# Kernel optimization log

Hardware: AMD Instinct MI355X
Metric: run time of the kernel (lower is better)

Reference implementation:

```python
import jax, jax.numpy as jnp
import numpy as np

IMG_DIM = 28 * 28


def _distmat(X):
    # D[i,j] = ||x_i||^2 - 2 x_i.x_j + ||x_j||^2
    r = jnp.sum(X * X, axis=1)
    a = X @ X.T
    return r[:, None] - 2.0 * a + r[None, :]


def _sigma_from_self(D, m):
    """Replicates sigma_estimation(X, X): median of the strict lower triangle of
    distmat(cat([X, X])), which is the 2x2 block-tiled matrix [[D,D],[D,D]].
    Its strict lower triangle multiset = full D (block 2,1) + 2x strict tril(D).
    Clamps: if med<=0 use mean; floor at 0.01. Detached (stop_gradient), matching
    the torch .detach().cpu().numpy() path."""
    mask = jnp.tril(jnp.ones((m, m), dtype=bool), -1)
    tril_inf = jnp.where(mask, D, jnp.inf)
    vals = jnp.concatenate([D.ravel(), tril_inf.ravel(), tril_inf.ravel()])
    s = jnp.sort(vals)  # inf padding sorts to the end
    k = 2 * m * m - m  # number of strict-lower-triangle entries of a 2m x 2m matrix
    if k % 2 == 0:
        med = 0.5 * (s[k // 2 - 1] + s[k // 2])  # np.median averages middles
    else:
        med = s[(k - 1) // 2]
    tri_sum = jnp.sum(jnp.where(mask, D, 0.0))
    mean_tri = (jnp.sum(D) + 2.0 * tri_sum) / k
    med = jnp.where(med <= 0.0, mean_tri, med)
    med = jnp.maximum(med, 0.01)
    return jax.lax.stop_gradient(med)


def _centered_kernel(D, sigma):
    # Kxc = Kx @ (I - ones/m)  ==  Kx - rowmean(Kx)
    K = jnp.exp(-D / (2.0 * sigma * sigma))
    return K - jnp.mean(K, axis=1, keepdims=True)


def _hsic_norm_from_kernels(Kxc, Kyc):
    Pxy = jnp.mean(Kxc * Kyc.T)
    Px = jnp.sqrt(jnp.mean(Kxc * Kxc.T))
    Py = jnp.sqrt(jnp.mean(Kyc * Kyc.T))
    return Pxy / (Px * Py)


def reference(x, y):
    x2 = x.reshape((-1, IMG_DIM))  # [m, 784]
    m = x2.shape[0]
    d = y.shape[-1]

    # hsic_normalized(x, y) with per-variable median sigma
    Dx = _distmat(x2)
    Dy = _distmat(y)
    Kx = _centered_kernel(Dx, _sigma_from_self(Dx, m))
    Ky = _centered_kernel(Dy, _sigma_from_self(Dy, m))
    mi_io = _hsic_norm_from_kernels(Kx, Ky)

    # Batched version of the nested loop over latent component pairs (i<j).
    # Per-column 1-D distance matrices: [d, m, m]
    yt = y.T  # [d, m]
    Dc = (yt[:, :, None] - yt[:, None, :]) ** 2
    sig = jax.vmap(lambda D: _sigma_from_self(D, m))(Dc)  # [d]
    Kc = jnp.exp(-Dc / (2.0 * sig * sig)[:, None, None])
    Kc = Kc - jnp.mean(Kc, axis=2, keepdims=True)  # centered, [d, m, m]

    # P[a,b] = mean(K_a * K_b^T)
    P = jnp.einsum('aij,bji->ab', Kc, Kc) / (m * m)
    diag = jnp.diagonal(P)
    norm = P / jnp.sqrt(diag[:, None] * diag[None, :])
    pair_mask = jnp.triu(jnp.ones((d, d), dtype=bool), 1)  # i < j
    mi_component_sum = jnp.sum(jnp.where(pair_mask, norm, 0.0))

    return -mi_io + mi_component_sum


def setup_inputs() -> dict:
    key = jax.random.key(0)
    kx, ky = jax.random.split(key)
    x = jax.random.normal(kx, (2048, 784), dtype=jnp.float32)
    y = jax.random.normal(ky, (2048, 10), dtype=jnp.float32)
    return {"x": x, "y": y}
```

## Files before the change

### kernel.cpp

```cpp
#include <hip/hip_runtime.h>
#include <math.h>

constexpr int Md   = 2048;
constexpr int NDIM = 784;
constexpr int DYC  = 10;
constexpr int MM   = Md * Md;
constexpr unsigned RANK_LO = 4193279u;
constexpr unsigned RANK_HI = 4193280u;
constexpr int NPROB = 12;
constexpr int NB    = 128;
constexpr int NBINS = 8192;

constexpr size_t OFF_DX     = 0;
constexpr size_t OFF_DY     = OFF_DX + (size_t)MM * 4;
constexpr size_t OFF_RX     = OFF_DY + (size_t)MM * 4;
constexpr size_t OFF_RY     = OFF_RX + Md * 8;
constexpr size_t OFF_RC     = OFF_RY + Md * 8;
constexpr size_t OFF_GACC   = OFF_RC + (size_t)DYC * Md * 8;
constexpr size_t OFF_HISTA  = OFF_GACC + 64 * 8;
constexpr size_t OFF_HISTB  = OFF_HISTA + (size_t)NPROB * NBINS * 4;
constexpr size_t OFF_JOBS   = OFF_HISTB + (size_t)NPROB * NBINS * 4;
constexpr size_t OFF_SELKEY = OFF_JOBS + NPROB * 5 * 4;
constexpr size_t OFF_Q      = OFF_SELKEY + NPROB * 2 * 4;
constexpr size_t OFF_RXN    = OFF_Q + NPROB * 4;
constexpr size_t OFF_YT     = OFF_RXN + Md * 4;
constexpr size_t OFF_RES    = OFF_YT + (size_t)DYC * Md * 4;
constexpr size_t WS_NEED    = OFF_RES + 70 * 8;
constexpr size_t ZERO_BASE  = OFF_GACC;
constexpr size_t ZERO_LEN   = OFF_JOBS - OFF_GACC;

typedef _Float16 f16x8 __attribute__((ext_vector_type(8)));
typedef _Float16 f16x4 __attribute__((ext_vector_type(4)));
typedef float    f32x16 __attribute__((ext_vector_type(16)));

__device__ __forceinline__ unsigned fkey(float v) {
  unsigned u = __float_as_uint(v);
  return (u & 0x80000000u) ? ~u : (u | 0x80000000u);
}
__device__ __forceinline__ float keyinv(unsigned k) {
  unsigned u = (k & 0x80000000u) ? (k ^ 0x80000000u) : ~k;
  return __uint_as_float(u);
}
__device__ __forceinline__ f16x8 ld8(const _Float16* p) {
  f16x4 lo = *(const f16x4*)p;
  f16x4 hi = *(const f16x4*)(p + 4);
  f16x8 r;
  r[0]=lo[0]; r[1]=lo[1]; r[2]=lo[2]; r[3]=lo[3];
  r[4]=hi[0]; r[5]=hi[1]; r[6]=hi[2]; r[7]=hi[3];
  return r;
}
__device__ __forceinline__ double waveReduceD(double v) {
  #pragma unroll
  for (int o = 32; o > 0; o >>= 1) v += __shfl_down(v, o, 64);
  return v;
}

__device__ __forceinline__ double blockReduceD(double v) {
  __shared__ double sred[4];
  v = waveReduceD(v);
  int lane = threadIdx.x & 63;
  int w    = threadIdx.x >> 6;
  __syncthreads();
  if (lane == 0) sred[w] = v;
  __syncthreads();
  double r = 0.0;
  if (threadIdx.x == 0) { r = sred[0] + sred[1] + sred[2] + sred[3]; }
  return r;
}

__global__ void fail_kernel(float* out) { if (threadIdx.x == 0) out[0] = 0.0f; }

__global__ void init_jobs_kernel(unsigned* __restrict__ jobs) {
  int p = threadIdx.x;
  if (p < NPROB) {
    jobs[p * 5 + 0] = 0u;
    jobs[p * 5 + 1] = RANK_LO;
    jobs[p * 5 + 2] = 0u;
    jobs[p * 5 + 3] = RANK_HI;
    jobs[p * 5 + 4] = 0u;
  }
}

__global__ __launch_bounds__(256) void transpose_y_kernel(const float* __restrict__ Y,
                                                          float* __restrict__ Yt) {
  int e = blockIdx.x * 256 + threadIdx.x;
  if (e < Md * DYC) {
    int i = e / DYC, c = e % DYC;
    Yt[c * Md + i] = Y[e];
  }
}

__global__ __launch_bounds__(256) void rownorm_kernel(const float* __restrict__ X,
                                                      float* __restrict__ rxn) {
  int i = blockIdx.x;
  double acc = 0.0;
  for (int k = threadIdx.x; k < NDIM; k += 256) {
    float v = X[i * NDIM + k];
    acc += (double)v * (double)v;
  }
  double r = blockReduceD(acc);
  if (threadIdx.x == 0) rxn[i] = (float)r;
}

__global__ __launch_bounds__(256) void distx_mfma(const float* __restrict__ X,
                                                  const float* __restrict__ rxn,
                                                  float* __restrict__ D) {
  __shared__ _Float16 Ah[64][68], Al[64][68], Bh[64][68], Bl[64][68];
  const int tid  = threadIdx.x;
  const int i0 = blockIdx.y * 64, j0 = blockIdx.x * 64;
  const int wave = tid >> 6, lane = tid & 63;
  const int wr = (wave >> 1) * 32, wc = (wave & 1) * 32;
  const int srow = tid >> 2;
  const int sseg = (tid & 3) * 8;

  f32x16 acc_hh = {}, acc_c1 = {}, acc_c2 = {};

  const float* Arow = X + (size_t)(i0 + srow) * NDIM;
  const float* Brow = X + (size_t)(j0 + srow) * NDIM;
  const int lrow = lane & 31;
  const int lko  = (lane >> 5) * 8;

  for (int k0 = 0; k0 < 800; k0 += 32) {
    float a[8], b[8];
    if (k0 + 32 <= NDIM) {
      float4 a4 = *(const float4*)(Arow + k0 + sseg);
      float4 a5 = *(const float4*)(Arow + k0 + sseg + 4);
      float4 b4 = *(const float4*)(Brow + k0 + sseg);
      float4 b5 = *(const float4*)(Brow + k0 + sseg + 4);
      a[0]=a4.x; a[1]=a4.y; a[2]=a4.z; a[3]=a4.w; a[4]=a5.x; a[5]=a5.y; a[6]=a5.z; a[7]=a5.w;
      b[0]=b4.x; b[1]=b4.y; b[2]=b4.z; b[3]=b4.w; b[4]=b5.x; b[5]=b5.y; b[6]=b5.z; b[7]=b5.w;
    } else {
      #pragma unroll
      for (int u = 0; u < 8; ++u) {
        int k = k0 + sseg + u;
        a[u] = (k < NDIM) ? Arow[k] : 0.0f;
        b[u] = (k < NDIM) ? Brow[k] : 0.0f;
      }
    }
    __syncthreads();
    #pragma unroll
    for (int half = 0; half < 2; ++half) {
      f16x4 vah, val_, vbh, vbl;
      #pragma unroll
      for (int u = 0; u < 4; ++u) {
        float av = a[half * 4 + u];
        _Float16 h = (_Float16)av;
        vah[u] = h; val_[u] = (_Float16)(av - (float)h);
        float bv = b[half * 4 + u];
        _Float16 g = (_Float16)bv;
        vbh[u] = g; vbl[u] = (_Float16)(bv - (float)g);
      }
      *(f16x4*)&Ah[srow][sseg + half * 4] = vah;
      *(f16x4*)&Al[srow][sseg + half * 4] = val_;
      *(f16x4*)&Bh[srow][sseg + half * 4] = vbh;
      *(f16x4*)&Bl[srow][sseg + half * 4] = vbl;
    }
    __syncthreads();
    #pragma unroll
    for (int ks = 0; ks < 2; ++ks) {
      int ko = ks * 16 + lko;
      f16x8 fah = ld8(&Ah[wr + lrow][ko]);
      f16x8 fal = ld8(&Al[wr + lrow][ko]);
      f16x8 fbh = ld8(&Bh[wc + lrow][ko]);
      f16x8 fbl = ld8(&Bl[wc + lrow][ko]);
      acc_hh = __builtin_amdgcn_mfma_f32_32x32x16_f16(fah, fbh, acc_hh, 0, 0, 0);
      acc_c1 = __builtin_amdgcn_mfma_f32_32x32x16_f16(fah, fbl, acc_c1, 0, 0, 0);
      acc_c2 = __builtin_amdgcn_mfma_f32_32x32x16_f16(fal, fbh, acc_c2, 0, 0, 0);
    }
  }
  int col = j0 + wc + (lane & 31);
  float rj = rxn[col];
  #pragma unroll
  for (int r = 0; r < 16; ++r) {
    int row = i0 + wr + (r & 3) + 8 * (r >> 2) + 4 * (lane >> 5);
    float t = rxn[row] + rj;
    float cc = acc_c1[r] + acc_c2[r];
    D[(size_t)row * Md + col] = fmaf(-2.0f, cc, fmaf(-2.0f, acc_hh[r], t));
  }
}

__global__ __launch_bounds__(256) void disty_kernel(const float* __restrict__ Y,
                                                    float* __restrict__ D) {
  __shared__ float Yi[64][10];
  __shared__ float Yj[64][10];
  int i0 = blockIdx.y * 64, j0 = blockIdx.x * 64;
  for (int t = threadIdx.x; t < 640; t += 256) {
    int r = t / 10, c = t % 10;
    Yi[r][c] = Y[(i0 + r) * DYC + c];
    Yj[r][c] = Y[(j0 + r) * DYC + c];
  }
  __syncthreads();
  int jj = threadIdx.x & 63;
  int ii0 = (threadIdx.x >> 6) * 16;
  float yj[10];
  #pragma unroll
  for (int c = 0; c < 10; ++c) yj[c] = Yj[jj][c];
  for (int r = 0; r < 16; ++r) {
    int ii = ii0 + r;
    float s = 0.f;
    #pragma unroll
    for (int c = 0; c < 10; ++c) { float d = Yi[ii][c] - yj[c]; s = fmaf(d, d, s); }
    D[(size_t)(i0 + ii) * Md + (j0 + jj)] = s;
  }
}

__global__ __launch_bounds__(256) void hist_kernel(const float* __restrict__ Dx,
                                                   const float* __restrict__ Dy,
                                                   const float* __restrict__ Yt,
                                                   unsigned* __restrict__ histA,
                                                   unsigned* __restrict__ histB,
                                                   const unsigned* __restrict__ jobs,
                                                   int level) {
  __shared__ unsigned lh[NBINS];
  __shared__ float ycol[Md];
  int prob = blockIdx.y;
  for (int b = threadIdx.x; b < NBINS; b += 256) lh[b] = 0;
  const float* Mptr = (prob == 0) ? Dx : (prob == 1 ? Dy : nullptr);
  if (prob >= 2) {
    const float* src = Yt + (size_t)(prob - 2) * Md;
    for (int i = threadIdx.x; i < Md; i += 256) ycol[i] = src[i];
  }
  __syncthreads();
  unsigned pfxL = jobs[prob * 5 + 0];
  unsigned pfxH = jobs[prob * 5 + 2];
  unsigned div  = jobs[prob * 5 + 4];
  unsigned* ghB = histB + prob * NBINS;
  for (int r = 0; r < Md / NB; ++r) {
    int i = blockIdx.x + r * NB;
    const float* row = Mptr ? (Mptr + (size_t)i * Md) : nullptr;
    float yi = Mptr ? 0.f : ycol[i];
    for (int j = threadIdx.x; j <= i; j += 256) {
      float v;
      if (Mptr) v = row[j];
      else { float d = yi - ycol[j]; v = d * d; }
      unsigned key = fkey(v);
      unsigned w = (j == i) ? 1u : 4u;
      if (level == 0) {
        atomicAdd(&lh[key >> 19], w);
      } else if (level == 1) {
        if ((key >> 19) == pfxL)             atomicAdd(&lh[(key >> 6) & 8191u], w);
        else if (div && (key >> 19) == pfxH) atomicAdd(&ghB[(key >> 6) & 8191u], w);
      } else {
        if ((key >> 6) == pfxL)              atomicAdd(&lh[key & 63u], w);
        else if (div && (key >> 6) == pfxH)  atomicAdd(&ghB[key & 63u], w);
      }
    }
  }
  __syncthreads();
  unsigned* ghA = histA + prob * NBINS;
  for (int b = threadIdx.x; b < NBINS; b += 256) {
    unsigned v = lh[b];
    if (v) atomicAdd(&ghA[b], v);
  }
}

__global__ __launch_bounds__(256) void select_kernel(unsigned* __restrict__ histA,
                                                     unsigned* __restrict__ histB,
                                                     unsigned* __restrict__ jobs,
                                                     unsigned* __restrict__ selkey,
                                                     int level) {
  __shared__ unsigned lhA[NBINS], lhB[NBINS];
  __shared__ unsigned psA[256], psB[256];
  int prob = blockIdx.x;
  int nbins = (level == 2) ? 64 : NBINS;
  int C = (nbins + 255) / 256;
  unsigned* ghA = histA + prob * NBINS;
  unsigned* ghB = histB + prob * NBINS;
  unsigned sA = 0, sB = 0;
  for (int k = 0; k < C; ++k) {
    int b = threadIdx.x * C + k;
    if (b < nbins) {
      unsigned v = ghA[b]; lhA[b] = v; sA += v;
      unsigned u = ghB[b]; lhB[b] = u; sB += u;
    }
  }
  psA[threadIdx.x] = sA; psB[threadIdx.x] = sB;
  __syncthreads();
  if (threadIdx.x == 0) {
    unsigned pfxL = jobs[prob * 5 + 0], remL = jobs[prob * 5 + 1];
    unsigned pfxH = jobs[prob * 5 + 2], remH = jobs[prob * 5 + 3];
    unsigned wasdiv = jobs[prob * 5 + 4];

    auto scan = [&](const unsigned* ps, const unsigned* lhp, unsigned r,
                    int& bin, unsigned& cum) {
      unsigned c = 0; int t = 0;
      for (; t < 255; ++t) { if (c + ps[t] > r) break; c += ps[t]; }
      int b = t * C;
      int be = b + C - 1; if (be > nbins - 1) be = nbins - 1;
      for (; b < be; ++b) { if (c + lhp[b] > r) break; c += lhp[b]; }
      bin = b; cum = c;
    };

    int bL; unsigned cL; scan(psA, lhA, remL, bL, cL);
    int bH; unsigned cH;
    unsigned div = wasdiv;
    if (!wasdiv) {
      scan(psA, lhA, remH, bH, cH);
      if (bH != bL) div = 1;
    } else {
      scan(psB, lhB, remH, bH, cH);
    }
    unsigned baseH = wasdiv ? pfxH : pfxL;
    if (level < 2) {
      jobs[prob * 5 + 0] = (level == 0) ? (unsigned)bL : ((pfxL << 13) | (unsigned)bL);
      jobs[prob * 5 + 2] = (level == 0) ? (unsigned)bH : ((baseH << 13) | (unsigned)bH);
      jobs[prob * 5 + 1] = remL - cL;
      jobs[prob * 5 + 3] = remH - cH;
      jobs[prob * 5 + 4] = div;
    } else {
      selkey[prob * 2 + 0] = (pfxL << 6) | (unsigned)bL;
      selkey[prob * 2 + 1] = (baseH << 6) | (unsigned)bH;
    }
  }
  __syncthreads();
  for (int b = threadIdx.x; b < nbins; b += 256) { ghA[b] = 0; ghB[b] = 0; }
}

__global__ void sigma2_kernel(const unsigned* __restrict__ selkey,
                              float* __restrict__ q) {
  int p = threadIdx.x;
  if (p < NPROB) {
    float med = 0.5f * (keyinv(selkey[p * 2]) + keyinv(selkey[p * 2 + 1]));
    med = fmaxf(med, 0.01f);
    q[p] = 2.0f * med * med;
  }
}

__global__ __launch_bounds__(256) void rowgrand_kernel(const float* __restrict__ Dx,
                                                       const float* __restrict__ Dy,
                                                       const float* __restrict__ q,
                                                       double* __restrict__ Rx,
                                                       double* __restrict__ Ry,
                                                       double* __restrict__ gacc) {
  __shared__ double red[3 * 4];
  const int wave = threadIdx.x >> 6, lane = threadIdx.x & 63;
  const float qx = q[0], qy = q[1];
  double gxx = 0, gxy = 0, gyy = 0;
  #pragma unroll
  for (int rr = 0; rr < 2; ++rr) {
    int i = blockIdx.x * 4 + wave + rr * 1024;
    const float4* rx4 = (const float4*)(Dx + (size_t)i * Md);
    const float4* ry4 = (const float4*)(Dy + (size_t)i * Md);
    double ax = 0, ay = 0;
    #pragma unroll
    for (int it = 0; it < 8; ++it) {
      float4 xv = rx4[it * 64 + lane];
      float4 yv = ry4[it * 64 + lane];
      #pragma unroll
      for (int u = 0; u < 4; ++u) {
        float xe = (u == 0) ? xv.x : (u == 1) ? xv.y : (u == 2) ? xv.z : xv.w;
        float ye = (u == 0) ? yv.x : (u == 1) ? yv.y : (u == 2) ? yv.z : yv.w;
        float ex = expm1f(-(xe / qx));
        float ey = expm1f(-(ye / qy));
        ax += (double)ex; ay += (double)ey;
        gxx += (double)ex * ex;
        gxy += (double)ex * ey;
        gyy += (double)ey * ey;
      }
    }
    ax = waveReduceD(ax);
    ay = waveReduceD(ay);
    if (lane == 0) { Rx[i] = ax; Ry[i] = ay; }
  }
  gxx = waveReduceD(gxx);
  gxy = waveReduceD(gxy);
  gyy = waveReduceD(gyy);
  if (lane == 0) { red[wave] = gxx; red[4 + wave] = gxy; red[8 + wave] = gyy; }
  __syncthreads();
  if (threadIdx.x == 0) {
    atomicAdd(&gacc[0], red[0] + red[1] + red[2] + red[3]);
    atomicAdd(&gacc[1], red[4] + red[5] + red[6] + red[7]);
    atomicAdd(&gacc[2], red[8] + red[9] + red[10] + red[11]);
  }
}

__global__ __launch_bounds__(256) void comp_rowsum_kernel(const float* __restrict__ Yt,
                                                          const float* __restrict__ q,
                                                          double* __restrict__ Rc) {
  const int wave = threadIdx.x >> 6, lane = threadIdx.x & 63;
  const int i = blockIdx.x * 4 + wave;
  float yi[10], ninv[10];
  #pragma unroll
  for (int c = 0; c < 10; ++c) { yi[c] = Yt[c * Md + i]; ninv[c] = -1.0f / q[2 + c]; }
  float facc[10] = {};
  #pragma unroll 2
  for (int it = 0; it < 8; ++it) {
    int j = it * 256 + lane * 4;
    #pragma unroll
    for (int c = 0; c < 10; ++c) {
      float4 v = *(const float4*)(Yt + c * Md + j);
      float d0 = yi[c] - v.x, d1 = yi[c] - v.y, d2 = yi[c] - v.z, d3 = yi[c] - v.w;
      facc[c] += __expf(d0 * d0 * ninv[c]) - 1.0f;
      facc[c] += __expf(d1 * d1 * ninv[c]) - 1.0f;
      facc[c] += __expf(d2 * d2 * ninv[c]) - 1.0f;
      facc[c] += __expf(d3 * d3 * ninv[c]) - 1.0f;
    }
  }
  #pragma unroll
  for (int c = 0; c < 10; ++c) {
    double r = waveReduceD((double)facc[c]);
    if (lane == 0) Rc[c * Md + i] = r;
  }
}

__global__ __launch_bounds__(256, 4) void comp_grand_kernel(const float* __restrict__ Yt,
                                                            const float* __restrict__ q,
                                                            double* __restrict__ gacc) {
  float ninv[10];
  #pragma unroll
  for (int c = 0; c < 10; ++c) ninv[c] = -1.0f / q[2 + c];
  int tid0 = blockIdx.x * 256 + threadIdx.x;
  int j = tid0 & 2047;
  float yj[10];
  #pragma unroll
  for (int c = 0; c < 10; ++c) yj[c] = Yt[c * Md + j];
  float facc[55];
  #pragma unroll
  for (int k = 0; k < 55; ++k) facc[k] = 0.0f;
  for (int i = tid0 >> 11; i < Md; i += 64) {
    float e[10];
    #pragma unroll
    for (int c = 0; c < 10; ++c) {
      float d = Yt[c * Md + i] - yj[c];
      e[c] = __expf(d * d * ninv[c]) - 1.0f;
    }
    int k = 0;
    #pragma unroll
    for (int a = 0; a < 10; ++a)
      #pragma unroll
      for (int b = a; b < 10; ++b) { facc[k] = fmaf(e[a], e[b], facc[k]); ++k; }
  }
  __shared__ double red[55 * 4];
  int lane = threadIdx.x & 63, w = threadIdx.x >> 6;
  #pragma unroll
  for (int k = 0; k < 55; ++k) {
    double v = waveReduceD((double)facc[k]);
    if (lane == 0) red[k * 4 + w] = v;
  }
  __syncthreads();
  for (int k = threadIdx.x; k < 55; k += 256) {
    double v = red[k * 4] + red[k * 4 + 1] + red[k * 4 + 2] + red[k * 4 + 3];
    atomicAdd(&gacc[3 + k], v);
  }
}

__global__ __launch_bounds__(256) void final_sums_kernel(const double* __restrict__ Rx,
                                                         const double* __restrict__ Ry,
                                                         const double* __restrict__ Rc,
                                                         double* __restrict__ res) {
  int k = blockIdx.x;
  double acc = 0.0;
  if (k < 5) {
    for (int i = threadIdx.x; i < Md; i += 256) {
      double a = Rx[i], b = Ry[i];
      acc += (k == 0) ? a : (k == 1) ? b : (k == 2) ? a * b : (k == 3) ? a * a : b * b;
    }
  } else if (k < 15) {
    const double* p = Rc + (size_t)(k - 5) * Md;
    for (int i = threadIdx.x; i < Md; i += 256) acc += p[i];
  } else {
    int kk = k - 15;
    int a = 0;
    while (kk >= 10 - a) { kk -= 10 - a; ++a; }
    int b = a + kk;
    const double* pa = Rc + (size_t)a * Md;
    const double* pb = Rc + (size_t)b * Md;
    for (int i = threadIdx.x; i < Md; i += 256) acc += pa[i] * pb[i];
  }
  double r = blockReduceD(acc);
  if (threadIdx.x == 0) res[k] = r;
}

__global__ void final_combine_kernel(const double* __restrict__ res,
                                     const double* __restrict__ gacc,
                                     float* __restrict__ out) {
  if (threadIdx.x != 0) return;
  const double m = (double)Md, m2 = m * m;
  double Gxx = gacc[0], Gxy = gacc[1], Gyy = gacc[2];
  double Sxy = Gxy - (2.0 / m) * res[2] + (res[0] * res[1]) / m2;
  double Sxx = Gxx - (2.0 / m) * res[3] + (res[0] * res[0]) / m2;
  double Syy = Gyy - (2.0 / m) * res[4] + (res[1] * res[1]) / m2;
  double mi_io = Sxy / sqrt(Sxx * Syy);

  double Sc[55], diag[10];
  int k = 0;
  for (int a = 0; a < 10; ++a)
    for (int b = a; b < 10; ++b) {
      double S = gacc[3 + k] - (2.0 / m) * res[15 + k] + (res[5 + a] * res[5 + b]) / m2;
      Sc[k] = S;
      if (a == b) diag[a] = S;
      ++k;
    }
  double comp = 0.0;
  k = 0;
  for (int a = 0; a < 10; ++a)
    for (int b = a; b < 10; ++b) {
      if (b > a) comp += Sc[k] / sqrt(diag[a] * diag[b]);
      ++k;
    }
  out[0] = (float)(-mi_io + comp);
}

extern "C" void kernel_launch(void* const* d_in, const int* in_sizes, int n_in,
                              void* d_out, int out_size, void* d_ws, size_t ws_size,
                              hipStream_t stream) {
  const float* X = (const float*)d_in[0];
  const float* Y = (const float*)d_in[1];
  float* out = (float*)d_out;
  char* ws = (char*)d_ws;

  if (ws_size < WS_NEED) {
    fail_kernel<<<1, 64, 0, stream>>>(out);
    return;
  }

  float*    Dx     = (float*)(ws + OFF_DX);
  float*    Dy     = (float*)(ws + OFF_DY);
  double*   Rx     = (double*)(ws + OFF_RX);
  double*   Ry     = (double*)(ws + OFF_RY);
  double*   Rc     = (double*)(ws + OFF_RC);
  double*   gacc   = (double*)(ws + OFF_GACC);
  unsigned* histA  = (unsigned*)(ws + OFF_HISTA);
  unsigned* histB  = (unsigned*)(ws + OFF_HISTB);
  unsigned* jobs   = (unsigned*)(ws + OFF_JOBS);
  unsigned* selkey = (unsigned*)(ws + OFF_SELKEY);
  float*    q      = (float*)(ws + OFF_Q);
  float*    rxn    = (float*)(ws + OFF_RXN);
  float*    Yt     = (float*)(ws + OFF_YT);
  double*   res    = (double*)(ws + OFF_RES);

  hipMemsetAsync(ws + ZERO_BASE, 0, ZERO_LEN, stream);
  init_jobs_kernel<<<1, 32, 0, stream>>>(jobs);
  transpose_y_kernel<<<80, 256, 0, stream>>>(Y, Yt);

  rownorm_kernel<<<Md, 256, 0, stream>>>(X, rxn);
  distx_mfma<<<dim3(32, 32), 256, 0, stream>>>(X, rxn, Dx);
  disty_kernel<<<dim3(32, 32), 256, 0, stream>>>(Y, Dy);

  for (int lvl = 0; lvl < 3; ++lvl) {
    hist_kernel<<<dim3(NB, NPROB), 256, 0, stream>>>(Dx, Dy, Yt, histA, histB, jobs, lvl);
    select_kernel<<<NPROB, 256, 0, stream>>>(histA, histB, jobs, selkey, lvl);
  }
  sigma2_kernel<<<1, 32, 0, stream>>>(selkey, q);

  rowgrand_kernel<<<256, 256, 0, stream>>>(Dx, Dy, q, Rx, Ry, gacc);
  comp_rowsum_kernel<<<512, 256, 0, stream>>>(Yt, q, Rc);
  comp_grand_kernel<<<512, 256, 0, stream>>>(Yt, q, gacc);
  final_sums_kernel<<<70, 256, 0, stream>>>(Rx, Ry, Rc, res);
  final_combine_kernel<<<1, 64, 0, stream>>>(res, gacc, out);
}
```

Baseline: 431.4 us.

## Fuse pipeline into fewer kernels with last-block selection and vectorized histogram

Merges the prep kernels (row norms, Y transpose, job init) into one launch and the two distance kernels into one grid. The select and sigma kernels are folded into the histogram kernel through a last-block-done counter, and the phase-3 and final kernels are merged the same way. The histogram loop now reads float4 vectors, and the histogram grid is doubled to 256 blocks per problem. The aim is to cut launch count and serialization gaps, at the cost of atomic completion counters and more complex control flow.

```diff
diff --git a/kernel.cpp b/kernel.cpp
--- a/kernel.cpp
+++ b/kernel.cpp
@@ -8,7 +8,7 @@
 constexpr unsigned RANK_LO = 4193279u;
 constexpr unsigned RANK_HI = 4193280u;
 constexpr int NPROB = 12;
-constexpr int NB    = 128;
+constexpr int NB    = 256;
 constexpr int NBINS = 8192;
 
 constexpr size_t OFF_DX     = 0;
@@ -19,13 +19,13 @@
 constexpr size_t OFF_GACC   = OFF_RC + (size_t)DYC * Md * 8;
 constexpr size_t OFF_HISTA  = OFF_GACC + 64 * 8;
 constexpr size_t OFF_HISTB  = OFF_HISTA + (size_t)NPROB * NBINS * 4;
-constexpr size_t OFF_JOBS   = OFF_HISTB + (size_t)NPROB * NBINS * 4;
-constexpr size_t OFF_SELKEY = OFF_JOBS + NPROB * 5 * 4;
-constexpr size_t OFF_Q      = OFF_SELKEY + NPROB * 2 * 4;
+constexpr size_t OFF_DONE   = OFF_HISTB + (size_t)NPROB * NBINS * 4;
+constexpr size_t OFF_RES    = OFF_DONE + 64 * 4;
+constexpr size_t OFF_JOBS   = OFF_RES + 72 * 8;
+constexpr size_t OFF_Q      = OFF_JOBS + NPROB * 5 * 4;
 constexpr size_t OFF_RXN    = OFF_Q + NPROB * 4;
 constexpr size_t OFF_YT     = OFF_RXN + Md * 4;
-constexpr size_t OFF_RES    = OFF_YT + (size_t)DYC * Md * 4;
-constexpr size_t WS_NEED    = OFF_RES + 70 * 8;
+constexpr size_t WS_NEED    = OFF_YT + (size_t)DYC * Md * 4;
 constexpr size_t ZERO_BASE  = OFF_GACC;
 constexpr size_t ZERO_LEN   = OFF_JOBS - OFF_GACC;
 
@@ -54,7 +54,6 @@
   for (int o = 32; o > 0; o >>= 1) v += __shfl_down(v, o, 64);
   return v;
 }
-
 __device__ __forceinline__ double blockReduceD(double v) {
   __shared__ double sred[4];
   v = waveReduceD(v);
@@ -70,44 +69,67 @@
 
 __global__ void fail_kernel(float* out) { if (threadIdx.x == 0) out[0] = 0.0f; }
 
-__global__ void init_jobs_kernel(unsigned* __restrict__ jobs) {
-  int p = threadIdx.x;
-  if (p < NPROB) {
-    jobs[p * 5 + 0] = 0u;
-    jobs[p * 5 + 1] = RANK_LO;
-    jobs[p * 5 + 2] = 0u;
-    jobs[p * 5 + 3] = RANK_HI;
-    jobs[p * 5 + 4] = 0u;
-  }
-}
-
-__global__ __launch_bounds__(256) void transpose_y_kernel(const float* __restrict__ Y,
-                                                          float* __restrict__ Yt) {
-  int e = blockIdx.x * 256 + threadIdx.x;
-  if (e < Md * DYC) {
-    int i = e / DYC, c = e % DYC;
-    Yt[c * Md + i] = Y[e];
-  }
-}
-
-__global__ __launch_bounds__(256) void rownorm_kernel(const float* __restrict__ X,
-                                                      float* __restrict__ rxn) {
-  int i = blockIdx.x;
-  double acc = 0.0;
-  for (int k = threadIdx.x; k < NDIM; k += 256) {
-    float v = X[i * NDIM + k];
-    acc += (double)v * (double)v;
-  }
-  double r = blockReduceD(acc);
-  if (threadIdx.x == 0) rxn[i] = (float)r;
-}
-
-__global__ __launch_bounds__(256) void distx_mfma(const float* __restrict__ X,
-                                                  const float* __restrict__ rxn,
-                                                  float* __restrict__ D) {
+__global__ __launch_bounds__(256) void prep_kernel(const float* __restrict__ X,
+                                                   const float* __restrict__ Y,
+                                                   float* __restrict__ rxn,
+                                                   float* __restrict__ Yt,
+                                                   unsigned* __restrict__ jobs) {
+  int bb = blockIdx.x;
+  if (bb < Md) {
+    double acc = 0.0;
+    for (int k = threadIdx.x; k < NDIM; k += 256) {
+      float v = X[bb * NDIM + k];
+      acc += (double)v * (double)v;
+    }
+    double r = blockReduceD(acc);
+    if (threadIdx.x == 0) rxn[bb] = (float)r;
+  } else if (bb < Md + 80) {
+    int e = (bb - Md) * 256 + threadIdx.x;
+    if (e < Md * DYC) {
+      int i = e / DYC, c = e % DYC;
+      Yt[c * Md + i] = Y[e];
+    }
+  } else {
+    int t = threadIdx.x;
+    if (t < NPROB * 5) {
+      int w = t % 5;
+      jobs[t] = (w == 1) ? RANK_LO : (w == 3) ? RANK_HI : 0u;
+    }
+  }
+}
+
+__global__ __launch_bounds__(256) void dist_kernel(const float* __restrict__ X,
+                                                   const float* __restrict__ Y,
+                                                   const float* __restrict__ rxn,
+                                                   float* __restrict__ Dx,
+                                                   float* __restrict__ Dy) {
   __shared__ _Float16 Ah[64][68], Al[64][68], Bh[64][68], Bl[64][68];
-  const int tid  = threadIdx.x;
+  __shared__ float Yi[64][10], Yj[64][10];
+  const int tid = threadIdx.x;
   const int i0 = blockIdx.y * 64, j0 = blockIdx.x * 64;
+
+  if (blockIdx.z == 1) {
+    for (int t = tid; t < 640; t += 256) {
+      int r = t / 10, c = t % 10;
+      Yi[r][c] = Y[(i0 + r) * DYC + c];
+      Yj[r][c] = Y[(j0 + r) * DYC + c];
+    }
+    __syncthreads();
+    int jj = tid & 63;
+    int ii0 = (tid >> 6) * 16;
+    float yj[10];
+    #pragma unroll
+    for (int c = 0; c < 10; ++c) yj[c] = Yj[jj][c];
+    for (int r = 0; r < 16; ++r) {
+      int ii = ii0 + r;
+      float s = 0.f;
+      #pragma unroll
+      for (int c = 0; c < 10; ++c) { float d = Yi[ii][c] - yj[c]; s = fmaf(d, d, s); }
+      Dy[(size_t)(i0 + ii) * Md + (j0 + jj)] = s;
+    }
+    return;
+  }
+
   const int wave = tid >> 6, lane = tid & 63;
   const int wr = (wave >> 1) * 32, wc = (wave & 1) * 32;
   const int srow = tid >> 2;
@@ -175,32 +197,7 @@
     int row = i0 + wr + (r & 3) + 8 * (r >> 2) + 4 * (lane >> 5);
     float t = rxn[row] + rj;
     float cc = acc_c1[r] + acc_c2[r];
-    D[(size_t)row * Md + col] = fmaf(-2.0f, cc, fmaf(-2.0f, acc_hh[r], t));
-  }
-}
-
-__global__ __launch_bounds__(256) void disty_kernel(const float* __restrict__ Y,
-                                                    float* __restrict__ D) {
-  __shared__ float Yi[64][10];
-  __shared__ float Yj[64][10];
-  int i0 = blockIdx.y * 64, j0 = blockIdx.x * 64;
-  for (int t = threadIdx.x; t < 640; t += 256) {
-    int r = t / 10, c = t % 10;
-    Yi[r][c] = Y[(i0 + r) * DYC + c];
-    Yj[r][c] = Y[(j0 + r) * DYC + c];
-  }
-  __syncthreads();
-  int jj = threadIdx.x & 63;
-  int ii0 = (threadIdx.x >> 6) * 16;
-  float yj[10];
-  #pragma unroll
-  for (int c = 0; c < 10; ++c) yj[c] = Yj[jj][c];
-  for (int r = 0; r < 16; ++r) {
-    int ii = ii0 + r;
-    float s = 0.f;
-    #pragma unroll
-    for (int c = 0; c < 10; ++c) { float d = Yi[ii][c] - yj[c]; s = fmaf(d, d, s); }
-    D[(size_t)(i0 + ii) * Md + (j0 + jj)] = s;
+    Dx[(size_t)row * Md + col] = fmaf(-2.0f, cc, fmaf(-2.0f, acc_hh[r], t));
   }
 }
 
@@ -209,7 +206,9 @@
                                                    const float* __restrict__ Yt,
                                                    unsigned* __restrict__ histA,
                                                    unsigned* __restrict__ histB,
-                                                   const unsigned* __restrict__ jobs,
+                                                   unsigned* __restrict__ jobs,
+                                                   unsigned* __restrict__ done,
+                                                   float* __restrict__ q,
                                                    int level) {
   __shared__ unsigned lh[NBINS];
   __shared__ float ycol[Md];
@@ -224,230 +223,263 @@
   unsigned pfxL = jobs[prob * 5 + 0];
   unsigned pfxH = jobs[prob * 5 + 2];
   unsigned div  = jobs[prob * 5 + 4];
+  unsigned* ghA = histA + prob * NBINS;
   unsigned* ghB = histB + prob * NBINS;
+
+  auto histo = [&](float v, unsigned w) {
+    unsigned key = fkey(v);
+    if (level == 0) {
+      atomicAdd(&lh[key >> 19], w);
+    } else if (level == 1) {
+      if ((key >> 19) == pfxL)             atomicAdd(&lh[(key >> 6) & 8191u], w);
+      else if (div && (key >> 19) == pfxH) atomicAdd(&ghB[(key >> 6) & 8191u], w);
+    } else {
+      if ((key >> 6) == pfxL)              atomicAdd(&lh[key & 63u], w);
+      else if (div && (key >> 6) == pfxH)  atomicAdd(&ghB[key & 63u], w);
+    }
+  };
+
   for (int r = 0; r < Md / NB; ++r) {
     int i = blockIdx.x + r * NB;
-    const float* row = Mptr ? (Mptr + (size_t)i * Md) : nullptr;
-    float yi = Mptr ? 0.f : ycol[i];
-    for (int j = threadIdx.x; j <= i; j += 256) {
-      float v;
-      if (Mptr) v = row[j];
-      else { float d = yi - ycol[j]; v = d * d; }
-      unsigned key = fkey(v);
-      unsigned w = (j == i) ? 1u : 4u;
-      if (level == 0) {
-        atomicAdd(&lh[key >> 19], w);
-      } else if (level == 1) {
-        if ((key >> 19) == pfxL)             atomicAdd(&lh[(key >> 6) & 8191u], w);
-        else if (div && (key >> 19) == pfxH) atomicAdd(&ghB[(key >> 6) & 8191u], w);
-      } else {
-        if ((key >> 6) == pfxL)              atomicAdd(&lh[key & 63u], w);
-        else if (div && (key >> 6) == pfxH)  atomicAdd(&ghB[key & 63u], w);
-      }
-    }
-  }
-  __syncthreads();
-  unsigned* ghA = histA + prob * NBINS;
+    int n = i + 1, ng = n >> 2, tail = n & 3;
+    if (Mptr) {
+      const float4* row4 = (const float4*)(Mptr + (size_t)i * Md);
+      for (int g = threadIdx.x; g < ng; g += 256) {
+        float4 v = row4[g];
+        int jb = g << 2;
+        histo(v.x, (jb == i) ? 1u : 4u);
+        histo(v.y, (jb + 1 == i) ? 1u : 4u);
+        histo(v.z, (jb + 2 == i) ? 1u : 4u);
+        histo(v.w, (jb + 3 == i) ? 1u : 4u);
+      }
+      if (threadIdx.x < tail) {
+        int j = (ng << 2) + threadIdx.x;
+        histo(Mptr[(size_t)i * Md + j], (j == i) ? 1u : 4u);
+      }
+    } else {
+      float yi = ycol[i];
+      for (int g = threadIdx.x; g < ng; g += 256) {
+        float4 y4 = *(const float4*)&ycol[g << 2];
+        int jb = g << 2;
+        float d0 = yi - y4.x, d1 = yi - y4.y, d2 = yi - y4.z, d3 = yi - y4.w;
+        histo(d0 * d0, (jb == i) ? 1u : 4u);
+        histo(d1 * d1, (jb + 1 == i) ? 1u : 4u);
+        histo(d2 * d2, (jb + 2 == i) ? 1u : 4u);
+        histo(d3 * d3, (jb + 3 == i) ? 1u : 4u);
+      }
+      if (threadIdx.x < tail) {
+        int j = (ng << 2) + threadIdx.x;
+        float d = yi - ycol[j];
+        histo(d * d, (j == i) ? 1u : 4u);
+      }
+    }
+  }
+  __syncthreads();
   for (int b = threadIdx.x; b < NBINS; b += 256) {
     unsigned v = lh[b];
     if (v) atomicAdd(&ghA[b], v);
   }
-}
-
-__global__ __launch_bounds__(256) void select_kernel(unsigned* __restrict__ histA,
-                                                     unsigned* __restrict__ histB,
-                                                     unsigned* __restrict__ jobs,
-                                                     unsigned* __restrict__ selkey,
-                                                     int level) {
-  __shared__ unsigned lhA[NBINS], lhB[NBINS];
-  __shared__ unsigned psA[256], psB[256];
-  int prob = blockIdx.x;
+  __threadfence();
+  __syncthreads();
+
+  unsigned* sel = (unsigned*)ycol;
+  if (threadIdx.x == 0) {
+    unsigned old = atomicAdd(&done[level * NPROB + prob], 1u);
+    sel[0] = (old == NB - 1) ? 1u : 0u;
+  }
+  __syncthreads();
+  if (!sel[0]) return;
+
+  unsigned* ps = sel + 8;
   int nbins = (level == 2) ? 64 : NBINS;
-  int C = (nbins + 255) / 256;
-  unsigned* ghA = histA + prob * NBINS;
-  unsigned* ghB = histB + prob * NBINS;
-  unsigned sA = 0, sB = 0;
-  for (int k = 0; k < C; ++k) {
-    int b = threadIdx.x * C + k;
-    if (b < nbins) {
-      unsigned v = ghA[b]; lhA[b] = v; sA += v;
-      unsigned u = ghB[b]; lhB[b] = u; sB += u;
-    }
-  }
-  psA[threadIdx.x] = sA; psB[threadIdx.x] = sB;
+  int C = (nbins > 256) ? (nbins / 256) : 1;
+  unsigned remL = jobs[prob * 5 + 1];
+  unsigned remH = jobs[prob * 5 + 3];
+  unsigned wasdiv = div;
+
+  auto scan = [&](unsigned r, int& bin, unsigned& cum) {
+    unsigned c = 0; int t = 0;
+    for (; t < 255; ++t) { if (c + ps[t] > r) break; c += ps[t]; }
+    int b = t * C;
+    int be = b + C - 1; if (be > nbins - 1) be = nbins - 1;
+    for (; b < be; ++b) { if (c + lh[b] > r) break; c += lh[b]; }
+    bin = b; cum = c;
+  };
+
+  for (int b = threadIdx.x; b < nbins; b += 256) lh[b] = atomicExch(&ghA[b], 0u);
+  __syncthreads();
+  {
+    unsigned s = 0;
+    for (int k2 = 0; k2 < C; ++k2) { int b = threadIdx.x * C + k2; if (b < nbins) s += lh[b]; }
+    ps[threadIdx.x] = s;
+  }
   __syncthreads();
   if (threadIdx.x == 0) {
-    unsigned pfxL = jobs[prob * 5 + 0], remL = jobs[prob * 5 + 1];
-    unsigned pfxH = jobs[prob * 5 + 2], remH = jobs[prob * 5 + 3];
-    unsigned wasdiv = jobs[prob * 5 + 4];
-
-    auto scan = [&](const unsigned* ps, const unsigned* lhp, unsigned r,
-                    int& bin, unsigned& cum) {
-      unsigned c = 0; int t = 0;
-      for (; t < 255; ++t) { if (c + ps[t] > r) break; c += ps[t]; }
-      int b = t * C;
-      int be = b + C - 1; if (be > nbins - 1) be = nbins - 1;
-      for (; b < be; ++b) { if (c + lhp[b] > r) break; c += lhp[b]; }
-      bin = b; cum = c;
-    };
-
-    int bL; unsigned cL; scan(psA, lhA, remL, bL, cL);
-    int bH; unsigned cH;
-    unsigned div = wasdiv;
+    int bL; unsigned cL; scan(remL, bL, cL);
+    sel[1] = (unsigned)bL; sel[2] = cL;
     if (!wasdiv) {
-      scan(psA, lhA, remH, bH, cH);
-      if (bH != bL) div = 1;
+      int bH; unsigned cH; scan(remH, bH, cH);
+      sel[3] = (unsigned)bH; sel[4] = cH;
+      sel[5] = (bH != bL) ? 1u : 0u;
     } else {
-      scan(psB, lhB, remH, bH, cH);
-    }
+      sel[5] = 1u;
+    }
+  }
+  __syncthreads();
+  if (wasdiv) {
+    for (int b = threadIdx.x; b < nbins; b += 256) lh[b] = atomicExch(&ghB[b], 0u);
+    __syncthreads();
+    unsigned s = 0;
+    for (int k2 = 0; k2 < C; ++k2) { int b = threadIdx.x * C + k2; if (b < nbins) s += lh[b]; }
+    ps[threadIdx.x] = s;
+    __syncthreads();
+    if (threadIdx.x == 0) {
+      int bH; unsigned cH; scan(remH, bH, cH);
+      sel[3] = (unsigned)bH; sel[4] = cH;
+    }
+    __syncthreads();
+  }
+  if (threadIdx.x == 0) {
+    unsigned bL = sel[1], cL = sel[2], bH = sel[3], cH = sel[4], ndiv = sel[5];
     unsigned baseH = wasdiv ? pfxH : pfxL;
     if (level < 2) {
-      jobs[prob * 5 + 0] = (level == 0) ? (unsigned)bL : ((pfxL << 13) | (unsigned)bL);
-      jobs[prob * 5 + 2] = (level == 0) ? (unsigned)bH : ((baseH << 13) | (unsigned)bH);
+      jobs[prob * 5 + 0] = (level == 0) ? bL : ((pfxL << 13) | bL);
+      jobs[prob * 5 + 2] = (level == 0) ? bH : ((baseH << 13) | bH);
       jobs[prob * 5 + 1] = remL - cL;
       jobs[prob * 5 + 3] = remH - cH;
-      jobs[prob * 5 + 4] = div;
+      jobs[prob * 5 + 4] = ndiv;
     } else {
-      selkey[prob * 2 + 0] = (pfxL << 6) | (unsigned)bL;
-      selkey[prob * 2 + 1] = (baseH << 6) | (unsigned)bH;
-    }
-  }
-  __syncthreads();
-  for (int b = threadIdx.x; b < nbins; b += 256) { ghA[b] = 0; ghB[b] = 0; }
-}
-
-__global__ void sigma2_kernel(const unsigned* __restrict__ selkey,
-                              float* __restrict__ q) {
-  int p = threadIdx.x;
-  if (p < NPROB) {
-    float med = 0.5f * (keyinv(selkey[p * 2]) + keyinv(selkey[p * 2 + 1]));
-    med = fmaxf(med, 0.01f);
-    q[p] = 2.0f * med * med;
-  }
-}
-
-__global__ __launch_bounds__(256) void rowgrand_kernel(const float* __restrict__ Dx,
-                                                       const float* __restrict__ Dy,
-                                                       const float* __restrict__ q,
-                                                       double* __restrict__ Rx,
-                                                       double* __restrict__ Ry,
-                                                       double* __restrict__ gacc) {
-  __shared__ double red[3 * 4];
+      unsigned keyL = (pfxL << 6) | bL;
+      unsigned keyH = (baseH << 6) | bH;
+      float med = 0.5f * (keyinv(keyL) + keyinv(keyH));
+      med = fmaxf(med, 0.01f);
+      q[prob] = 2.0f * med * med;
+    }
+  }
+}
+
+__global__ __launch_bounds__(256, 4) void phase3_kernel(const float* __restrict__ Dx,
+                                                        const float* __restrict__ Dy,
+                                                        const float* __restrict__ Yt,
+                                                        const float* __restrict__ q,
+                                                        double* __restrict__ Rx,
+                                                        double* __restrict__ Ry,
+                                                        double* __restrict__ Rc,
+                                                        double* __restrict__ gacc) {
+  __shared__ double shred[224];
   const int wave = threadIdx.x >> 6, lane = threadIdx.x & 63;
-  const float qx = q[0], qy = q[1];
-  double gxx = 0, gxy = 0, gyy = 0;
-  #pragma unroll
-  for (int rr = 0; rr < 2; ++rr) {
-    int i = blockIdx.x * 4 + wave + rr * 1024;
-    const float4* rx4 = (const float4*)(Dx + (size_t)i * Md);
-    const float4* ry4 = (const float4*)(Dy + (size_t)i * Md);
-    double ax = 0, ay = 0;
-    #pragma unroll
+  int bb = blockIdx.x;
+
+  if (bb < 256) {
+    const float qx = q[0], qy = q[1];
+    double gxx = 0, gxy = 0, gyy = 0;
+    #pragma unroll
+    for (int rr = 0; rr < 2; ++rr) {
+      int i = bb * 4 + wave + rr * 1024;
+      const float4* rx4 = (const float4*)(Dx + (size_t)i * Md);
+      const float4* ry4 = (const float4*)(Dy + (size_t)i * Md);
+      double ax = 0, ay = 0;
+      #pragma unroll
+      for (int it = 0; it < 8; ++it) {
+        float4 xv = rx4[it * 64 + lane];
+        float4 yv = ry4[it * 64 + lane];
+        #pragma unroll
+        for (int u = 0; u < 4; ++u) {
+          float xe = (u == 0) ? xv.x : (u == 1) ? xv.y : (u == 2) ? xv.z : xv.w;
+          float ye = (u == 0) ? yv.x : (u == 1) ? yv.y : (u == 2) ? yv.z : yv.w;
+          float ex = expm1f(-(xe / qx));
+          float ey = expm1f(-(ye / qy));
+          ax += (double)ex; ay += (double)ey;
+          gxx += (double)ex * ex;
+          gxy += (double)ex * ey;
+          gyy += (double)ey * ey;
+        }
+      }
+      ax = waveReduceD(ax);
+      ay = waveReduceD(ay);
+      if (lane == 0) { Rx[i] = ax; Ry[i] = ay; }
+    }
+    gxx = waveReduceD(gxx);
+    gxy = waveReduceD(gxy);
+    gyy = waveReduceD(gyy);
+    if (lane == 0) { shred[wave] = gxx; shred[4 + wave] = gxy; shred[8 + wave] = gyy; }
+    __syncthreads();
+    if (threadIdx.x == 0) {
+      atomicAdd(&gacc[0], shred[0] + shred[1] + shred[2] + shred[3]);
+      atomicAdd(&gacc[1], shred[4] + shred[5] + shred[6] + shred[7]);
+      atomicAdd(&gacc[2], shred[8] + shred[9] + shred[10] + shred[11]);
+    }
+  } else if (bb < 768) {
+    int i = (bb - 256) * 4 + wave;
+    float yi[10], ninv[10];
+    #pragma unroll
+    for (int c = 0; c < 10; ++c) { yi[c] = Yt[c * Md + i]; ninv[c] = -1.0f / q[2 + c]; }
+    float facc[10] = {};
+    #pragma unroll 2
     for (int it = 0; it < 8; ++it) {
-      float4 xv = rx4[it * 64 + lane];
-      float4 yv = ry4[it * 64 + lane];
-      #pragma unroll
-      for (int u = 0; u < 4; ++u) {
-        float xe = (u == 0) ? xv.x : (u == 1) ? xv.y : (u == 2) ? xv.z : xv.w;
-        float ye = (u == 0) ? yv.x : (u == 1) ? yv.y : (u == 2) ? yv.z : yv.w;
-        float ex = expm1f(-(xe / qx));
-        float ey = expm1f(-(ye / qy));
-        ax += (double)ex; ay += (double)ey;
-        gxx += (double)ex * ex;
-        gxy += (double)ex * ey;
-        gyy += (double)ey * ey;
-      }
-    }
-    ax = waveReduceD(ax);
-    ay = waveReduceD(ay);
-    if (lane == 0) { Rx[i] = ax; Ry[i] = ay; }
-  }
-  gxx = waveReduceD(gxx);
-  gxy = waveReduceD(gxy);
-  gyy = waveReduceD(gyy);
-  if (lane == 0) { red[wave] = gxx; red[4 + wave] = gxy; red[8 + wave] = gyy; }
-  __syncthreads();
-  if (threadIdx.x == 0) {
-    atomicAdd(&gacc[0], red[0] + red[1] + red[2] + red[3]);
-    atomicAdd(&gacc[1], red[4] + red[5] + red[6] + red[7]);
-    atomicAdd(&gacc[2], red[8] + red[9] + red[10] + red[11]);
-  }
-}
-
-__global__ __launch_bounds__(256) void comp_rowsum_kernel(const float* __restrict__ Yt,
-                                                          const float* __restrict__ q,
-                                                          double* __restrict__ Rc) {
-  const int wave = threadIdx.x >> 6, lane = threadIdx.x & 63;
-  const int i = blockIdx.x * 4 + wave;
-  float yi[10], ninv[10];
-  #pragma unroll
-  for (int c = 0; c < 10; ++c) { yi[c] = Yt[c * Md + i]; ninv[c] = -1.0f / q[2 + c]; }
-  float facc[10] = {};
-  #pragma unroll 2
-  for (int it = 0; it < 8; ++it) {
-    int j = it * 256 + lane * 4;
+      int j = it * 256 + lane * 4;
+      #pragma unroll
+      for (int c = 0; c < 10; ++c) {
+        float4 v = *(const float4*)(Yt + c * Md + j);
+        float d0 = yi[c] - v.x, d1 = yi[c] - v.y, d2 = yi[c] - v.z, d3 = yi[c] - v.w;
+        facc[c] += __expf(d0 * d0 * ninv[c]) - 1.0f;
+        facc[c] += __expf(d1 * d1 * ninv[c]) - 1.0f;
+        facc[c] += __expf(d2 * d2 * ninv[c]) - 1.0f;
+        facc[c] += __expf(d3 * d3 * ninv[c]) - 1.0f;
+      }
+    }
     #pragma unroll
     for (int c = 0; c < 10; ++c) {
-      float4 v = *(const float4*)(Yt + c * Md + j);
-      float d0 = yi[c] - v.x, d1 = yi[c] - v.y, d2 = yi[c] - v.z, d3 = yi[c] - v.w;
-      facc[c] += __expf(d0 * d0 * ninv[c]) - 1.0f;
-      facc[c] += __expf(d1 * d1 * ninv[c]) - 1.0f;
-      facc[c] += __expf(d2 * d2 * ninv[c]) - 1.0f;
-      facc[c] += __expf(d3 * d3 * ninv[c]) - 1.0f;
-    }
-  }
-  #pragma unroll
-  for (int c = 0; c < 10; ++c) {
-    double r = waveReduceD((double)facc[c]);
-    if (lane == 0) Rc[c * Md + i] = r;
-  }
-}
-
-__global__ __launch_bounds__(256, 4) void comp_grand_kernel(const float* __restrict__ Yt,
-                                                            const float* __restrict__ q,
-                                                            double* __restrict__ gacc) {
-  float ninv[10];
-  #pragma unroll
-  for (int c = 0; c < 10; ++c) ninv[c] = -1.0f / q[2 + c];
-  int tid0 = blockIdx.x * 256 + threadIdx.x;
-  int j = tid0 & 2047;
-  float yj[10];
-  #pragma unroll
-  for (int c = 0; c < 10; ++c) yj[c] = Yt[c * Md + j];
-  float facc[55];
-  #pragma unroll
-  for (int k = 0; k < 55; ++k) facc[k] = 0.0f;
-  for (int i = tid0 >> 11; i < Md; i += 64) {
-    float e[10];
-    #pragma unroll
-    for (int c = 0; c < 10; ++c) {
-      float d = Yt[c * Md + i] - yj[c];
-      e[c] = __expf(d * d * ninv[c]) - 1.0f;
-    }
-    int k = 0;
-    #pragma unroll
-    for (int a = 0; a < 10; ++a)
-      #pragma unroll
-      for (int b = a; b < 10; ++b) { facc[k] = fmaf(e[a], e[b], facc[k]); ++k; }
-  }
-  __shared__ double red[55 * 4];
-  int lane = threadIdx.x & 63, w = threadIdx.x >> 6;
-  #pragma unroll
-  for (int k = 0; k < 55; ++k) {
-    double v = waveReduceD((double)facc[k]);
-    if (lane == 0) red[k * 4 + w] = v;
-  }
-  __syncthreads();
-  for (int k = threadIdx.x; k < 55; k += 256) {
-    double v = red[k * 4] + red[k * 4 + 1] + red[k * 4 + 2] + red[k * 4 + 3];
-    atomicAdd(&gacc[3 + k], v);
-  }
-}
-
-__global__ __launch_bounds__(256) void final_sums_kernel(const double* __restrict__ Rx,
-                                                         const double* __restrict__ Ry,
-                                                         const double* __restrict__ Rc,
-                                                         double* __restrict__ res) {
+      double r = waveReduceD((double)facc[c]);
+      if (lane == 0) Rc[c * Md + i] = r;
+    }
+  } else {
+    float ninv[10];
+    #pragma unroll
+    for (int c = 0; c < 10; ++c) ninv[c] = -1.0f / q[2 + c];
+    int tid0 = (bb - 768) * 256 + threadIdx.x;
+    int j = tid0 & 2047;
+    float yj[10];
+    #pragma unroll
+    for (int c = 0; c < 10; ++c) yj[c] = Yt[c * Md + j];
+    float facc[55];
+    #pragma unroll
+    for (int k = 0; k < 55; ++k) facc[k] = 0.0f;
+    for (int i = tid0 >> 11; i < Md; i += 64) {
+      float e[10];
+      #pragma unroll
+      for (int c = 0; c < 10; ++c) {
+        float d = Yt[c * Md + i] - yj[c];
+        e[c] = __expf(d * d * ninv[c]) - 1.0f;
+      }
+      int k = 0;
+      #pragma unroll
+      for (int a = 0; a < 10; ++a)
+        #pragma unroll
+        for (int b = a; b < 10; ++b) { facc[k] = fmaf(e[a], e[b], facc[k]); ++k; }
+    }
+    #pragma unroll
+    for (int k = 0; k < 55; ++k) {
+      double v = waveReduceD((double)facc[k]);
+      if (lane == 0) shred[k * 4 + wave] = v;
+    }
+    __syncthreads();
+    for (int k = threadIdx.x; k < 55; k += 256) {
+      double v = shred[k * 4] + shred[k * 4 + 1] + shred[k * 4 + 2] + shred[k * 4 + 3];
+      atomicAdd(&gacc[3 + k], v);
+    }
+  }
+}
+
+__global__ __launch_bounds__(256) void final_kernel(const double* __restrict__ Rx,
+                                                    const double* __restrict__ Ry,
+                                                    const double* __restrict__ Rc,
+                                                    const double* __restrict__ gacc,
+                                                    double* __restrict__ res,
+                                                    unsigned* __restrict__ done,
+                                                    float* __restrict__ out) {
+  __shared__ double sres[70];
+  __shared__ unsigned sflag;
   int k = blockIdx.x;
   double acc = 0.0;
   if (k < 5) {
@@ -468,37 +500,43 @@
     for (int i = threadIdx.x; i < Md; i += 256) acc += pa[i] * pb[i];
   }
   double r = blockReduceD(acc);
-  if (threadIdx.x == 0) res[k] = r;
-}
-
-__global__ void final_combine_kernel(const double* __restrict__ res,
-                                     const double* __restrict__ gacc,
-                                     float* __restrict__ out) {
-  if (threadIdx.x != 0) return;
-  const double m = (double)Md, m2 = m * m;
-  double Gxx = gacc[0], Gxy = gacc[1], Gyy = gacc[2];
-  double Sxy = Gxy - (2.0 / m) * res[2] + (res[0] * res[1]) / m2;
-  double Sxx = Gxx - (2.0 / m) * res[3] + (res[0] * res[0]) / m2;
-  double Syy = Gyy - (2.0 / m) * res[4] + (res[1] * res[1]) / m2;
-  double mi_io = Sxy / sqrt(Sxx * Syy);
-
-  double Sc[55], diag[10];
-  int k = 0;
-  for (int a = 0; a < 10; ++a)
-    for (int b = a; b < 10; ++b) {
-      double S = gacc[3 + k] - (2.0 / m) * res[15 + k] + (res[5 + a] * res[5 + b]) / m2;
-      Sc[k] = S;
-      if (a == b) diag[a] = S;
-      ++k;
-    }
-  double comp = 0.0;
-  k = 0;
-  for (int a = 0; a < 10; ++a)
-    for (int b = a; b < 10; ++b) {
-      if (b > a) comp += Sc[k] / sqrt(diag[a] * diag[b]);
-      ++k;
-    }
-  out[0] = (float)(-mi_io + comp);
+  if (threadIdx.x == 0) {
+    atomicAdd(&res[k], r);
+    __threadfence();
+    unsigned old = atomicAdd(&done[36], 1u);
+    sflag = (old == 69) ? 1u : 0u;
+  }
+  __syncthreads();
+  if (!sflag) return;
+
+  if (threadIdx.x < 70) sres[threadIdx.x] = atomicAdd(&res[threadIdx.x], 0.0);
+  __syncthreads();
+  if (threadIdx.x == 0) {
+    const double m = (double)Md, m2 = m * m;
+    double Gxx = gacc[0], Gxy = gacc[1], Gyy = gacc[2];
+    double Sxy = Gxy - (2.0 / m) * sres[2] + (sres[0] * sres[1]) / m2;
+    double Sxx = Gxx - (2.0 / m) * sres[3] + (sres[0] * sres[0]) / m2;
+    double Syy = Gyy - (2.0 / m) * sres[4] + (sres[1] * sres[1]) / m2;
+    double mi_io = Sxy / sqrt(Sxx * Syy);
+
+    double Sc[55], diag[10];
+    int kk = 0;
+    for (int a = 0; a < 10; ++a)
+      for (int b = a; b < 10; ++b) {
+        double S = gacc[3 + kk] - (2.0 / m) * sres[15 + kk] + (sres[5 + a] * sres[5 + b]) / m2;
+        Sc[kk] = S;
+        if (a == b) diag[a] = S;
+        ++kk;
+      }
+    double comp = 0.0;
+    kk = 0;
+    for (int a = 0; a < 10; ++a)
+      for (int b = a; b < 10; ++b) {
+        if (b > a) comp += Sc[kk] / sqrt(diag[a] * diag[b]);
+        ++kk;
+      }
+    out[0] = (float)(-mi_io + comp);
+  }
 }
 
 extern "C" void kernel_launch(void* const* d_in, const int* in_sizes, int n_in,
@@ -514,38 +552,29 @@
     return;
   }
 
-  float*    Dx     = (float*)(ws + OFF_DX);
-  float*    Dy     = (float*)(ws + OFF_DY);
-  double*   Rx     = (double*)(ws + OFF_RX);
-  double*   Ry     = (double*)(ws + OFF_RY);
-  double*   Rc     = (double*)(ws + OFF_RC);
-  double*   gacc   = (double*)(ws + OFF_GACC);
-  unsigned* histA  = (unsigned*)(ws + OFF_HISTA);
-  unsigned* histB  = (unsigned*)(ws + OFF_HISTB);
-  unsigned* jobs   = (unsigned*)(ws + OFF_JOBS);
-  unsigned* selkey = (unsigned*)(ws + OFF_SELKEY);
-  float*    q      = (float*)(ws + OFF_Q);
-  float*    rxn    = (float*)(ws + OFF_RXN);
-  float*    Yt     = (float*)(ws + OFF_YT);
-  double*   res    = (double*)(ws + OFF_RES);
+  float*    Dx    = (float*)(ws + OFF_DX);
+  float*    Dy    = (float*)(ws + OFF_DY);
+  double*   Rx    = (double*)(ws + OFF_RX);
+  double*   Ry    = (double*)(ws + OFF_RY);
+  double*   Rc    = (double*)(ws + OFF_RC);
+  double*   gacc  = (double*)(ws + OFF_GACC);
+  unsigned* histA = (unsigned*)(ws + OFF_HISTA);
+  unsigned* histB = (unsigned*)(ws + OFF_HISTB);
+  unsigned* done  = (unsigned*)(ws + OFF_DONE);
+  double*   res   = (double*)(ws + OFF_RES);
+  unsigned* jobs  = (unsigned*)(ws + OFF_JOBS);
+  float*    q     = (float*)(ws + OFF_Q);
+  float*    rxn   = (float*)(ws + OFF_RXN);
+  float*    Yt    = (float*)(ws + OFF_YT);
 
   hipMemsetAsync(ws + ZERO_BASE, 0, ZERO_LEN, stream);
-  init_jobs_kernel<<<1, 32, 0, stream>>>(jobs);
-  transpose_y_kernel<<<80, 256, 0, stream>>>(Y, Yt);
-
-  rownorm_kernel<<<Md, 256, 0, stream>>>(X, rxn);
-  distx_mfma<<<dim3(32, 32), 256, 0, stream>>>(X, rxn, Dx);
-  disty_kernel<<<dim3(32, 32), 256, 0, stream>>>(Y, Dy);
-
-  for (int lvl = 0; lvl < 3; ++lvl) {
-    hist_kernel<<<dim3(NB, NPROB), 256, 0, stream>>>(Dx, Dy, Yt, histA, histB, jobs, lvl);
-    select_kernel<<<NPROB, 256, 0, stream>>>(histA, histB, jobs, selkey, lvl);
-  }
-  sigma2_kernel<<<1, 32, 0, stream>>>(selkey, q);
-
-  rowgrand_kernel<<<256, 256, 0, stream>>>(Dx, Dy, q, Rx, Ry, gacc);
-  comp_rowsum_kernel<<<512, 256, 0, stream>>>(Yt, q, Rc);
-  comp_grand_kernel<<<512, 256, 0, stream>>>(Yt, q, gacc);
-  final_sums_kernel<<<70, 256, 0, stream>>>(Rx, Ry, Rc, res);
-  final_combine_kernel<<<1, 64, 0, stream>>>(res, gacc, out);
-}
+  prep_kernel<<<Md + 80 + 1, 256, 0, stream>>>(X, Y, rxn, Yt, jobs);
+  dist_kernel<<<dim3(32, 32, 2), 256, 0, stream>>>(X, Y, rxn, Dx, Dy);
+
+  for (int lvl = 0; lvl < 3; ++lvl)
+    hist_kernel<<<dim3(NB, NPROB), 256, 0, stream>>>(Dx, Dy, Yt, histA, histB,
+                                                     jobs, done, q, lvl);
+
+  phase3_kernel<<<1280, 256, 0, stream>>>(Dx, Dy, Yt, q, Rx, Ry, Rc, gacc);
+  final_kernel<<<70, 256, 0, stream>>>(Rx, Ry, Rc, gacc, res, done, out);
+}
```

Result: slower. 917.6 us (+112.7%).
